# Performance work log

Measured on AMD Instinct MI355X. Metric: run time of the kernel, lower is better.

The kernel has to match this reference:

```python
import jax, jax.numpy as jnp
import numpy as np

B_SZ, T_A, T_B, EMB, HID = 16, 1024, 1024, 768, 1024

def setup_inputs() -> dict:
    key = jax.random.key(0)
    kA, kB, k1, k2 = jax.random.split(key, 4)
    s1 = 1.0 / np.sqrt(EMB)
    s2 = 1.0 / np.sqrt(HID)
    return {
        "A": jax.random.normal(kA, (B_SZ, T_A, EMB), jnp.float32),
        "B": jax.random.normal(kB, (B_SZ, T_B, EMB), jnp.float32),
        "W1": jax.random.normal(k1, (EMB, HID), jnp.float32) * s1,
        "b1": jnp.zeros((HID,), jnp.float32),
        "W2": jax.random.normal(k2, (HID, HID), jnp.float32) * s2,
        "b2": jnp.zeros((HID,), jnp.float32),
    }

def _mlp(x, W1, b1, W2, b2):
    # Linear -> ReLU -> Linear -> ReLU (dropout omitted / eval mode)
    h = jax.nn.relu(x @ W1 + b1)
    return jax.nn.relu(h @ W2 + b2)

def reference(A, B, W1, b1, W2, b2):
    f_A = _mlp(A, W1, b1, W2, b2)             # (bs, ta, h)
    f_B = _mlp(B, W1, b1, W2, b2)             # (bs, tb, h)
    e = jnp.einsum("bah,bch->bac", f_A, f_B)  # (bs, ta, tb)
    beta = jnp.einsum("bac,bce->bae", jax.nn.softmax(e, axis=-1), B)
    alpha = jnp.einsum("bca,bae->bce",
                       jax.nn.softmax(e, axis=1).transpose(0, 2, 1)[:, :, :] * 1.0,
                       A) if False else jnp.einsum(
        "bca,bae->bce", jax.nn.softmax(e.transpose(0, 2, 1), axis=-1), A)
    return beta, alpha
```

## Files before the change

kernel.cpp:

```cpp
#include <hip/hip_runtime.h>
#include <cstdint>


#define L2E 1.4426950408889634f

typedef _Float16 half8 __attribute__((ext_vector_type(8)));
typedef _Float16 half4v __attribute__((ext_vector_type(4)));
typedef float f32x4 __attribute__((ext_vector_type(4)));

__device__ __forceinline__ void gl_lds16(const void* g, void* l) {
  __builtin_amdgcn_global_load_lds(
      (const __attribute__((address_space(1))) unsigned int*)g,
      (__attribute__((address_space(3))) unsigned int*)l, 16, 0, 0);
}

template<int K, bool BIASRELU, bool STATS, typename OutT>
__global__ __launch_bounds__(512, 2)
void gemm_k(const _Float16* __restrict__ X, const _Float16* __restrict__ Y,
            const float* __restrict__ bias, OutT* __restrict__ C, int N,
            long xbs, long ybs, long cbs, int gm, int gn, int gz,
            float* __restrict__ prm, float* __restrict__ prs,
            float* __restrict__ pcm, float* __restrict__ pcs,
            const _Float16* __restrict__ X2, const _Float16* __restrict__ Y2,
            OutT* __restrict__ C2, int shalf)
{
  constexpr int NS = K / 32;
  __shared__ __align__(16) _Float16 sm[65536];
  const int t = threadIdx.x;
  const int lane = t & 63, w = t >> 6;
  const int wr = w >> 2, wc = w & 3;
  const int lm = lane & 15, g = lane >> 4;

  const int id = blockIdx.x;
  const int c = id & 7;
  int s0 = id >> 3;
  if (shalf && s0 >= shalf) { s0 -= shalf; X = X2; Y = Y2; C = C2; }
  int m, n, bz;
  if (gz == 1) {
    int q = s0 / gn;
    n = s0 - q * gn;
    m = c * (gm >> 3) + q;
    bz = 0;
  } else {
    int tpb = gm * gn;
    int bq = s0 / tpb;
    bz = c * (gz >> 3) + bq;
    int r = s0 - bq * tpb;
    m = r / gn;
    n = r - m * gn;
  }
  const int m0 = m * 256, n0 = n * 256;

  X += (size_t)bz * xbs;
  Y += (size_t)bz * ybs;
  C += (size_t)bz * cbs;

  const _Float16* ag[2]; const _Float16* bg[2];
  _Float16* al[2]; _Float16* bl[2];
#pragma unroll
  for (int j = 0; j < 2; ++j) {
    int ci = j * 512 + t;
    int lr = ci >> 3, p = ci & 7;
    int cc = p ^ (lr & 7);
    int r = lr * 2 + (cc >> 2);
    int kb = (cc & 3) * 8;
    ag[j] = X + (size_t)(m0 + r) * K + kb;
    bg[j] = Y + (size_t)(n0 + r) * K + kb;
    al[j] = sm + ci * 8;
    bl[j] = sm + 8192 + ci * 8;
  }

  int aoff[8], boff[4];
#pragma unroll
  for (int mi = 0; mi < 8; ++mi) {
    int r = wr * 128 + mi * 16 + lm;
    int lr = r >> 1;
    aoff[mi] = lr * 64 + ((((lm & 1) << 2) + g) ^ (lr & 7)) * 8;
  }
#pragma unroll
  for (int ni = 0; ni < 4; ++ni) {
    int r = wc * 64 + ni * 16 + lm;
    int lr = r >> 1;
    boff[ni] = lr * 64 + ((((lm & 1) << 2) + g) ^ (lr & 7)) * 8;
  }

  f32x4 acc[8][4] = {};

#define STAGE_(ss) { \
    const int sb_ = ((ss) & 3) * 16384; \
    const int kt_ = (ss) * 32; \
    gl_lds16(ag[0] + kt_, al[0] + sb_); \
    gl_lds16(ag[1] + kt_, al[1] + sb_); \
    gl_lds16(bg[0] + kt_, bl[0] + sb_); \
    gl_lds16(bg[1] + kt_, bl[1] + sb_); }

#define SLOT_(ss, VM) { \
    asm volatile("s_waitcnt vmcnt(" #VM ")" ::: "memory"); \
    __builtin_amdgcn_s_barrier(); \
    const _Float16* ab_ = sm + ((ss) & 3) * 16384; \
    const _Float16* bb_ = ab_ + 8192; \
    half8 af[8]; half8 bf[4]; \
    _Pragma("unroll") \
    for (int mi = 0; mi < 8; ++mi) af[mi] = *(const half8*)(ab_ + aoff[mi]); \
    _Pragma("unroll") \
    for (int ni = 0; ni < 4; ++ni) bf[ni] = *(const half8*)(bb_ + boff[ni]); \
    if ((ss) + 3 < NS) STAGE_((ss) + 3); \
    __builtin_amdgcn_s_setprio(1); \
    _Pragma("unroll") \
    for (int mi = 0; mi < 8; ++mi) \
      _Pragma("unroll") \
      for (int ni = 0; ni < 4; ++ni) \
        acc[mi][ni] = __builtin_amdgcn_mfma_f32_16x16x32_f16(af[mi], bf[ni], acc[mi][ni], 0, 0, 0); \
    __builtin_amdgcn_s_setprio(0); }

  STAGE_(0); STAGE_(1); STAGE_(2);
  for (int ss = 0; ss < NS - 2; ++ss) SLOT_(ss, 8);
  SLOT_(NS - 2, 4);
  SLOT_(NS - 1, 0);
#undef STAGE_
#undef SLOT_

#pragma unroll
  for (int mi = 0; mi < 8; ++mi) {
    const int rb = m0 + wr * 128 + mi * 16 + g * 4;
#pragma unroll
    for (int ni = 0; ni < 4; ++ni) {
      const int col = n0 + wc * 64 + ni * 16 + lm;
      float bv = 0.f;
      if constexpr (BIASRELU) bv = bias[col];
#pragma unroll
      for (int q = 0; q < 4; ++q) {
        float v = acc[mi][ni][q] + bv;
        if constexpr (BIASRELU) v = fmaxf(v, 0.f);
        C[(size_t)(rb + q) * N + col] = (OutT)v;
      }
    }
  }

  if constexpr (STATS) {
    __syncthreads();
    float* sRm = (float*)sm;
    float* sRs = sRm + 1024;
    float* sCm = sRs + 1024;
    float* sCs = sCm + 512;

#pragma unroll
    for (int mi = 0; mi < 8; ++mi) {
#pragma unroll
      for (int q = 0; q < 4; ++q) {
        float mloc = fmaxf(fmaxf(acc[mi][0][q], acc[mi][1][q]),
                           fmaxf(acc[mi][2][q], acc[mi][3][q]));
#pragma unroll
        for (int msk = 1; msk < 16; msk <<= 1)
          mloc = fmaxf(mloc, __shfl_xor(mloc, msk));
        float sl = 0.f;
#pragma unroll
        for (int ni = 0; ni < 4; ++ni)
          sl += exp2f((acc[mi][ni][q] - mloc) * L2E);
#pragma unroll
        for (int msk = 1; msk < 16; msk <<= 1)
          sl += __shfl_xor(sl, msk);
        if (lm == 0) {
          int r = wr * 128 + mi * 16 + g * 4 + q;
          sRm[wc * 256 + r] = mloc;
          sRs[wc * 256 + r] = sl;
        }
      }
    }
#pragma unroll
    for (int ni = 0; ni < 4; ++ni) {
      float mloc = -3.0e38f;
#pragma unroll
      for (int mi = 0; mi < 8; ++mi)
#pragma unroll
        for (int q = 0; q < 4; ++q)
          mloc = fmaxf(mloc, acc[mi][ni][q]);
      mloc = fmaxf(mloc, __shfl_xor(mloc, 16));
      mloc = fmaxf(mloc, __shfl_xor(mloc, 32));
      float sl = 0.f;
#pragma unroll
      for (int mi = 0; mi < 8; ++mi)
#pragma unroll
        for (int q = 0; q < 4; ++q)
          sl += exp2f((acc[mi][ni][q] - mloc) * L2E);
      sl += __shfl_xor(sl, 16);
      sl += __shfl_xor(sl, 32);
      if (g == 0) {
        int cl = wc * 64 + ni * 16 + lm;
        sCm[wr * 256 + cl] = mloc;
        sCs[wr * 256 + cl] = sl;
      }
    }
    __syncthreads();
    if (t < 256) {
      float M = sRm[t];
#pragma unroll
      for (int j = 1; j < 4; ++j) M = fmaxf(M, sRm[j * 256 + t]);
      float S = 0.f;
#pragma unroll
      for (int j = 0; j < 4; ++j)
        S += sRs[j * 256 + t] * exp2f((sRm[j * 256 + t] - M) * L2E);
      size_t o = ((size_t)bz * 4 + n) * 1024 + m0 + t;
      prm[o] = M;
      prs[o] = S;
    } else {
      int u = t - 256;
      float M = fmaxf(sCm[u], sCm[256 + u]);
      float S = sCs[u] * exp2f((sCm[u] - M) * L2E) +
                sCs[256 + u] * exp2f((sCm[256 + u] - M) * L2E);
      size_t o = ((size_t)bz * 4 + m) * 1024 + n0 + u;
      pcm[o] = M;
      pcs[o] = S;
    }
  }
}

__global__ __launch_bounds__(256)
void softmax_apply(const float* __restrict__ e,
                   const float* __restrict__ prm, const float* __restrict__ prs,
                   const float* __restrict__ pcm, const float* __restrict__ pcs,
                   _Float16* __restrict__ P, _Float16* __restrict__ PT)
{
  __shared__ _Float16 tl[64][65];
  __shared__ float sRm[64], sRi[64], sCm[64], sCi[64];
  const int bz = blockIdx.z;
  const int r0 = blockIdx.y * 64, c0 = blockIdx.x * 64;
  const size_t bo = (size_t)bz * 1048576;
  const int t = threadIdx.x;

  if (t < 128) {
    const int isCol = t >> 6;
    const int u = t & 63;
    const float* pm = isCol ? pcm : prm;
    const float* ps = isCol ? pcs : prs;
    const int pos = (isCol ? c0 : r0) + u;
    float mj[4], sj[4];
#pragma unroll
    for (int j = 0; j < 4; ++j) {
      size_t o = ((size_t)bz * 4 + j) * 1024 + pos;
      mj[j] = pm[o];
      sj[j] = ps[o];
    }
    float M = -3.0e38f;
#pragma unroll
    for (int j = 0; j < 4; ++j) M = fmaxf(M, mj[j]);
    float S = 0.f;
#pragma unroll
    for (int j = 0; j < 4; ++j) S += sj[j] * exp2f((mj[j] - M) * L2E);
    if (isCol) { sCm[u] = M; sCi[u] = 1.f / S; }
    else       { sRm[u] = M; sRi[u] = 1.f / S; }
  }
  __syncthreads();

#pragma unroll
  for (int p = 0; p < 4; ++p) {
    int idx = p * 256 + t;
    int row = idx >> 4, col4 = (idx & 15) * 4;
    float4 v = *(const float4*)(e + bo + (size_t)(r0 + row) * 1024 + c0 + col4);
    float vv[4] = {v.x, v.y, v.z, v.w};
    const float mrow = sRm[row];
    const float irow = sRi[row];
    half4v op;
#pragma unroll
    for (int j = 0; j < 4; ++j) {
      op[j] = (_Float16)(exp2f((vv[j] - mrow) * L2E) * irow);
      tl[col4 + j][row] = (_Float16)(exp2f((vv[j] - sCm[col4 + j]) * L2E) * sCi[col4 + j]);
    }
    *(half4v*)(P + bo + (size_t)(r0 + row) * 1024 + c0 + col4) = op;
  }
  __syncthreads();
#pragma unroll
  for (int p = 0; p < 4; ++p) {
    int idx = p * 256 + t;
    int trow = idx >> 4, tcol4 = (idx & 15) * 4;
    half4v ov;
#pragma unroll
    for (int j = 0; j < 4; ++j) ov[j] = tl[trow][tcol4 + j];
    *(half4v*)(PT + bo + (size_t)(c0 + trow) * 1024 + r0 + tcol4) = ov;
  }
}

__global__ __launch_bounds__(256)
void transpose_cvt(const float* __restrict__ in1, _Float16* __restrict__ out1,
                   const float* __restrict__ in2, _Float16* __restrict__ out2,
                   int R, int C, int nb)
{
  __shared__ float tl[32][33];
  int z = blockIdx.z;
  const float* in = in1;
  _Float16* out = out1;
  if (z >= nb) { z -= nb; in = in2; out = out2; }
  const size_t bo = (size_t)z * R * C;
  int x = blockIdx.x * 32 + threadIdx.x;
  int y0 = blockIdx.y * 32;
  for (int i = threadIdx.y; i < 32; i += 8)
    tl[i][threadIdx.x] = in[bo + (size_t)(y0 + i) * C + x];
  __syncthreads();
  int xo = y0 + threadIdx.x;
  int c0 = blockIdx.x * 32;
  for (int i = threadIdx.y; i < 32; i += 8)
    out[bo + (size_t)(c0 + i) * R + xo] = (_Float16)tl[threadIdx.x][i];
}

__global__ __launch_bounds__(256)
void cvt_f16_2(const float* __restrict__ inA, const float* __restrict__ inB,
               _Float16* __restrict__ oA, _Float16* __restrict__ oB, int n4)
{
  int i = blockIdx.x * 256 + threadIdx.x;
  const float* in = inA;
  _Float16* out = oA;
  if (i >= n4) { i -= n4; in = inB; out = oB; }
  float4 v = ((const float4*)in)[i];
  half4v o;
  o[0] = (_Float16)v.x; o[1] = (_Float16)v.y; o[2] = (_Float16)v.z; o[3] = (_Float16)v.w;
  ((half4v*)out)[i] = o;
}

extern "C" void kernel_launch(void* const* d_in, const int* in_sizes, int n_in,
                              void* d_out, int out_size, void* d_ws, size_t ws_size,
                              hipStream_t stream)
{
  const float* A  = (const float*)d_in[0];
  const float* B  = (const float*)d_in[1];
  const float* W1 = (const float*)d_in[2];
  const float* b1 = (const float*)d_in[3];
  const float* W2 = (const float*)d_in[4];
  const float* b2 = (const float*)d_in[5];
  float* out = (float*)d_out;

  char* ws = (char*)d_ws;
  _Float16* Af  = (_Float16*)(ws + 0);
  _Float16* Bf  = (_Float16*)(ws + 25165824);
  _Float16* W1t = (_Float16*)(ws + 50331648);
  _Float16* W2t = (_Float16*)(ws + 51904512);
  float*    prm = (float*)   (ws + 50331648);
  float*    prs = (float*)   (ws + 50331648 + 524288);
  float*    pcm = (float*)   (ws + 50331648 + 1048576);
  float*    pcs = (float*)   (ws + 50331648 + 1572864);
  _Float16* fAB = (_Float16*)(ws + 54001664);
  _Float16* P   = (_Float16*)(ws + 54001664);
  _Float16* PT  = (_Float16*)(ws + 87556096);
  _Float16* h   = (_Float16*)(ws + 121110528);
  float*    e   = (float*)   (ws + 121110528);
  _Float16* fA = fAB;
  _Float16* fB = fAB + 16777216;
  _Float16* At = Af;
  _Float16* Bt = Bf;

  dim3 blk(256);
  dim3 blk5(512);
  dim3 tblk(32, 8);

  cvt_f16_2<<<24576, blk, 0, stream>>>(A, B, Af, Bf, 3145728);
  transpose_cvt<<<dim3(32, 24, 1), tblk, 0, stream>>>(W1, W1t, nullptr, nullptr, 768, 1024, 1);
  transpose_cvt<<<dim3(32, 32, 1), tblk, 0, stream>>>(W2, W2t, nullptr, nullptr, 1024, 1024, 1);

  gemm_k<768, true, false, _Float16><<<512, blk5, 0, stream>>>(
      Af, W1t, b1, h, 1024, 0, 0, 0, 128, 4, 1,
      nullptr, nullptr, nullptr, nullptr, nullptr, nullptr, nullptr, 0);
  transpose_cvt<<<dim3(24, 32, 32), tblk, 0, stream>>>(A, At, B, Bt, 1024, 768, 16);
  gemm_k<1024, true, false, _Float16><<<512, blk5, 0, stream>>>(
      h, W2t, b2, fAB, 1024, 0, 0, 0, 128, 4, 1,
      nullptr, nullptr, nullptr, nullptr, nullptr, nullptr, nullptr, 0);

  gemm_k<1024, false, true, float><<<256, blk5, 0, stream>>>(
      fA, fB, nullptr, e, 1024, 1048576L, 1048576L, 1048576L, 4, 4, 16,
      prm, prs, pcm, pcs, nullptr, nullptr, nullptr, 0);

  softmax_apply<<<dim3(16, 16, 16), blk, 0, stream>>>(e, prm, prs, pcm, pcs, P, PT);

  gemm_k<1024, false, false, float><<<384, blk5, 0, stream>>>(
      P, Bt, nullptr, out, 768, 1048576L, 786432L, 786432L, 4, 3, 16,
      nullptr, nullptr, nullptr, nullptr, PT, At, out + 12582912, 24);
}
```

Baseline: 508.9 us.

## Split GEMM K-slot into two half-phases interleaving LDS reads, prefetch and MFMA

Restructures each pipeline slot of the fp16 GEMM main loop into two halves. The first half-block of A fragments is read, half of the next stage's global-to-LDS loads are issued, and its MFMAs run. Then the second A half is read, the remaining loads are issued, and the vmcnt wait is moved to the end of the slot. This is meant to spread global loads and LDS reads across the MFMA work, in a ping-pong style schedule, and to lower register pressure from holding all eight A fragments at once. In exchange it adds extra barriers per slot and changes the wait counts and loop tail, which risks stalls or hazards from the buffer-reuse ordering.

```diff
diff --git a/kernel.cpp b/kernel.cpp
--- a/kernel.cpp
+++ b/kernel.cpp
@@ -95,27 +95,48 @@
     gl_lds16(bg[1] + kt_, bl[1] + sb_); }
 
 #define SLOT_(ss, VM) { \
+    const _Float16* ab_ = sm + ((ss) & 3) * 16384; \
+    const _Float16* bb_ = ab_ + 8192; \
+    const int sb_ = (((ss) + 3) & 3) * 16384; \
+    const int kt_ = ((ss) + 3) * 32; \
+    const bool st_ = (ss) + 3 < NS; \
+    half8 afA[4], bf[4], afB[4]; \
+    _Pragma("unroll") \
+    for (int mi = 0; mi < 4; ++mi) afA[mi] = *(const half8*)(ab_ + aoff[mi]); \
+    _Pragma("unroll") \
+    for (int ni = 0; ni < 4; ++ni) bf[ni] = *(const half8*)(bb_ + boff[ni]); \
+    if (st_) { gl_lds16(ag[0] + kt_, al[0] + sb_); \
+               gl_lds16(ag[1] + kt_, al[1] + sb_); } \
+    __builtin_amdgcn_s_barrier(); \
+    __builtin_amdgcn_s_setprio(1); \
+    _Pragma("unroll") \
+    for (int mi = 0; mi < 4; ++mi) \
+      _Pragma("unroll") \
+      for (int ni = 0; ni < 4; ++ni) \
+        acc[mi][ni] = __builtin_amdgcn_mfma_f32_16x16x32_f16(afA[mi], bf[ni], acc[mi][ni], 0, 0, 0); \
+    __builtin_amdgcn_s_setprio(0); \
+    __builtin_amdgcn_s_barrier(); \
+    _Pragma("unroll") \
+    for (int mi = 0; mi < 4; ++mi) afB[mi] = *(const half8*)(ab_ + aoff[4 + mi]); \
+    if (st_) { gl_lds16(bg[0] + kt_, bl[0] + sb_); \
+               gl_lds16(bg[1] + kt_, bl[1] + sb_); } \
     asm volatile("s_waitcnt vmcnt(" #VM ")" ::: "memory"); \
     __builtin_amdgcn_s_barrier(); \
-    const _Float16* ab_ = sm + ((ss) & 3) * 16384; \
-    const _Float16* bb_ = ab_ + 8192; \
-    half8 af[8]; half8 bf[4]; \
-    _Pragma("unroll") \
-    for (int mi = 0; mi < 8; ++mi) af[mi] = *(const half8*)(ab_ + aoff[mi]); \
-    _Pragma("unroll") \
-    for (int ni = 0; ni < 4; ++ni) bf[ni] = *(const half8*)(bb_ + boff[ni]); \
-    if ((ss) + 3 < NS) STAGE_((ss) + 3); \
     __builtin_amdgcn_s_setprio(1); \
     _Pragma("unroll") \
-    for (int mi = 0; mi < 8; ++mi) \
+    for (int mi = 0; mi < 4; ++mi) \
       _Pragma("unroll") \
       for (int ni = 0; ni < 4; ++ni) \
-        acc[mi][ni] = __builtin_amdgcn_mfma_f32_16x16x32_f16(af[mi], bf[ni], acc[mi][ni], 0, 0, 0); \
-    __builtin_amdgcn_s_setprio(0); }
+        acc[4 + mi][ni] = __builtin_amdgcn_mfma_f32_16x16x32_f16(afB[mi], bf[ni], acc[4 + mi][ni], 0, 0, 0); \
+    __builtin_amdgcn_s_setprio(0); \
+    __builtin_amdgcn_s_barrier(); }
 
   STAGE_(0); STAGE_(1); STAGE_(2);
-  for (int ss = 0; ss < NS - 2; ++ss) SLOT_(ss, 8);
-  SLOT_(NS - 2, 4);
+  asm volatile("s_waitcnt vmcnt(8)" ::: "memory");
+  __builtin_amdgcn_s_barrier();
+  for (int ss = 0; ss < NS - 3; ++ss) SLOT_(ss, 8);
+  SLOT_(NS - 3, 4);
+  SLOT_(NS - 2, 0);
   SLOT_(NS - 1, 0);
 #undef STAGE_
 #undef SLOT_
```

Result: no change. 506.4 us (-0.5%).

## Double-buffer LDS fragment reads in registers to overlap with MFMA compute

Applied to the files above, without the earlier changes.

Restructures the GEMM main loop so each window issues the ds_read_b128 loads for the next k-slice into a second register fragment set, then runs MFMAs on the current set. LDS reads use inline asm with precomputed byte addresses, and explicit waitcnt plus sched_barrier fences control ordering. The goal is to hide LDS read latency behind matrix-core work instead of stalling before each slot's MFMAs. The cost is a second set of A/B fragment registers, which raises register pressure under the 512x2 launch bounds, and hand-written wait counts that must match the prefetch depth.

```diff
diff --git a/kernel.cpp b/kernel.cpp
--- a/kernel.cpp
+++ b/kernel.cpp
@@ -12,6 +12,16 @@
   __builtin_amdgcn_global_load_lds(
       (const __attribute__((address_space(1))) unsigned int*)g,
       (__attribute__((address_space(3))) unsigned int*)l, 16, 0, 0);
+}
+
+__device__ __forceinline__ unsigned lds_addr(const void* p) {
+  return (unsigned)(uintptr_t)(const __attribute__((address_space(3))) void*)p;
+}
+
+__device__ __forceinline__ half8 ds_read_b128a(unsigned addr) {
+  f32x4 r;
+  asm volatile("ds_read_b128 %0, %1" : "=v"(r) : "v"(addr));
+  return __builtin_bit_cast(half8, r);
 }
 
 template<int K, bool BIASRELU, bool STATS, typename OutT>
@@ -70,18 +80,19 @@
     bl[j] = sm + 8192 + ci * 8;
   }
 
-  int aoff[8], boff[4];
+  const unsigned smb = lds_addr(sm);
+  unsigned abyte[8], bbyte[4];
 #pragma unroll
   for (int mi = 0; mi < 8; ++mi) {
     int r = wr * 128 + mi * 16 + lm;
     int lr = r >> 1;
-    aoff[mi] = lr * 64 + ((((lm & 1) << 2) + g) ^ (lr & 7)) * 8;
+    abyte[mi] = smb + (unsigned)(lr * 64 + ((((lm & 1) << 2) + g) ^ (lr & 7)) * 8) * 2;
   }
 #pragma unroll
   for (int ni = 0; ni < 4; ++ni) {
     int r = wc * 64 + ni * 16 + lm;
     int lr = r >> 1;
-    boff[ni] = lr * 64 + ((((lm & 1) << 2) + g) ^ (lr & 7)) * 8;
+    bbyte[ni] = smb + 16384u + (unsigned)(lr * 64 + ((((lm & 1) << 2) + g) ^ (lr & 7)) * 8) * 2;
   }
 
   f32x4 acc[8][4] = {};
@@ -94,31 +105,54 @@
     gl_lds16(bg[0] + kt_, bl[0] + sb_); \
     gl_lds16(bg[1] + kt_, bl[1] + sb_); }
 
-#define SLOT_(ss, VM) { \
-    asm volatile("s_waitcnt vmcnt(" #VM ")" ::: "memory"); \
-    __builtin_amdgcn_s_barrier(); \
-    const _Float16* ab_ = sm + ((ss) & 3) * 16384; \
-    const _Float16* bb_ = ab_ + 8192; \
-    half8 af[8]; half8 bf[4]; \
+#define READS_(ss, AF, BF) { \
+    const unsigned sbb_ = (unsigned)(((ss) & 3) * 32768); \
     _Pragma("unroll") \
-    for (int mi = 0; mi < 8; ++mi) af[mi] = *(const half8*)(ab_ + aoff[mi]); \
+    for (int mi = 0; mi < 8; ++mi) AF[mi] = ds_read_b128a(abyte[mi] + sbb_); \
     _Pragma("unroll") \
-    for (int ni = 0; ni < 4; ++ni) bf[ni] = *(const half8*)(bb_ + boff[ni]); \
-    if ((ss) + 3 < NS) STAGE_((ss) + 3); \
+    for (int ni = 0; ni < 4; ++ni) BF[ni] = ds_read_b128a(bbyte[ni] + sbb_); }
+
+#define MFMAS_(AF, BF) { \
     __builtin_amdgcn_s_setprio(1); \
     _Pragma("unroll") \
     for (int mi = 0; mi < 8; ++mi) \
       _Pragma("unroll") \
       for (int ni = 0; ni < 4; ++ni) \
-        acc[mi][ni] = __builtin_amdgcn_mfma_f32_16x16x32_f16(af[mi], bf[ni], acc[mi][ni], 0, 0, 0); \
+        acc[mi][ni] = __builtin_amdgcn_mfma_f32_16x16x32_f16(AF[mi], BF[ni], acc[mi][ni], 0, 0, 0); \
     __builtin_amdgcn_s_setprio(0); }
 
+#define WINDOW_(ww, VM, CA, CB, NA, NB) { \
+    asm volatile("s_waitcnt vmcnt(" #VM ")" ::: "memory"); \
+    __builtin_amdgcn_s_barrier(); \
+    asm volatile("s_waitcnt lgkmcnt(0)" ::: "memory"); \
+    __builtin_amdgcn_sched_barrier(0); \
+    READS_((ww) + 1, NA, NB); \
+    if ((ww) + 3 < NS) STAGE_((ww) + 3); \
+    MFMAS_(CA, CB); }
+
+  half8 a0[8], b0[4], a1[8], b1[4];
+
   STAGE_(0); STAGE_(1); STAGE_(2);
-  for (int ss = 0; ss < NS - 2; ++ss) SLOT_(ss, 8);
-  SLOT_(NS - 2, 4);
-  SLOT_(NS - 1, 0);
+  asm volatile("s_waitcnt vmcnt(8)" ::: "memory");
+  __builtin_amdgcn_s_barrier();
+  READS_(0, a0, b0);
+
+  for (int ww = 0; ww + 3 < NS; ww += 2) {
+    WINDOW_(ww,     4, a0, b0, a1, b1);
+    WINDOW_(ww + 1, 4, a1, b1, a0, b0);
+  }
+  WINDOW_(NS - 2, 0, a0, b0, a1, b1);
+  {
+    asm volatile("s_waitcnt vmcnt(0)" ::: "memory");
+    __builtin_amdgcn_s_barrier();
+    asm volatile("s_waitcnt lgkmcnt(0)" ::: "memory");
+    __builtin_amdgcn_sched_barrier(0);
+    MFMAS_(a1, b1);
+  }
 #undef STAGE_
-#undef SLOT_
+#undef READS_
+#undef MFMAS_
+#undef WINDOW_
 
 #pragma unroll
   for (int mi = 0; mi < 8; ++mi) {
```

New measurement: 537.5 us. 5.6% more time.
